# Optimization experiments

Hardware: AMD Instinct MI355X
Metric: run time of the kernel (lower is better)

The kernel has to match this reference:

```python
import jax, jax.numpy as jnp
import numpy as np

B = 8192
D = 512          # hidden_dim
OBS_EMB = 256
COMM = 128
N_ACT = 4
N_LAYERS = 2
D_INNER = 2 * D
D_STATE = 16
DT_RANK = D // 16  # 32
D_CONV = 4
EPS = 1e-5


def _xavier(k, shape):
    s = jnp.sqrt(2.0 / (shape[-2] + shape[-1]))
    return jax.random.normal(k, shape, jnp.float32) * s


def setup_inputs() -> dict:
    ks = jax.random.split(jax.random.key(0), 16)
    p = {}
    p['obs'] = jax.random.normal(ks[0], (B, 75), jnp.float32)
    p['comm_in'] = jax.random.normal(ks[1], (B, COMM), jnp.float32)
    # obs encoder: Conv2d(3->32, k=3, valid) + Linear(288->256)
    p['conv_w'] = jax.random.normal(ks[2], (32, 3, 3, 3), jnp.float32) * jnp.sqrt(2.0 / 27.0)
    p['conv_b'] = jnp.zeros((32,), jnp.float32)
    p['enc_w'] = _xavier(ks[3], (288, OBS_EMB))
    p['enc_b'] = jnp.zeros((OBS_EMB,), jnp.float32)
    p['proj_w'] = _xavier(ks[4], (OBS_EMB + COMM, D))
    p['proj_b'] = jnp.zeros((D,), jnp.float32)
    # Mamba stack params (stacked over layers)
    p['norm_w'] = jnp.ones((N_LAYERS, D), jnp.float32)
    p['in_proj_w'] = _xavier(ks[5], (N_LAYERS, D, 2 * D_INNER))
    p['conv1d_w'] = jax.random.normal(ks[6], (N_LAYERS, D_INNER, D_CONV), jnp.float32) / jnp.sqrt(D_CONV)
    p['conv1d_b'] = jnp.zeros((N_LAYERS, D_INNER), jnp.float32)
    p['x_proj_w'] = _xavier(ks[7], (N_LAYERS, D_INNER, DT_RANK + 2 * D_STATE))
    p['dt_proj_w'] = _xavier(ks[8], (N_LAYERS, DT_RANK, D_INNER))
    p['dt_proj_b'] = jnp.full((N_LAYERS, D_INNER), jnp.log(jnp.expm1(0.01)), jnp.float32)  # dt ~ 0.01
    p['A_log'] = jnp.log(jnp.broadcast_to(jnp.arange(1, D_STATE + 1, dtype=jnp.float32), (N_LAYERS, D_INNER, D_STATE)))
    p['D_param'] = jnp.ones((N_LAYERS, D_INNER), jnp.float32)
    p['out_proj_w'] = _xavier(ks[9], (N_LAYERS, D_INNER, D))
    p['final_norm_w'] = jnp.ones((D,), jnp.float32)
    # output heads
    p['act_w'] = _xavier(ks[10], (D, N_ACT)); p['act_b'] = jnp.zeros((N_ACT,), jnp.float32)
    p['comm_w'] = _xavier(ks[11], (D, COMM)); p['comm_b'] = jnp.zeros((COMM,), jnp.float32)
    p['val_w'] = _xavier(ks[12], (D, 1)); p['val_b'] = jnp.zeros((1,), jnp.float32)
    return p


def _rmsnorm(x, w):
    return x * jax.lax.rsqrt(jnp.mean(x * x, axis=-1, keepdims=True) + EPS) * w


def _mamba_block(u, Wi, cw, cb, Wx, Wdt, bdt, Alog, Dp, Wo):
    # u: (B, L, D) -> (B, L, D)
    Bsz, L, _ = u.shape
    d_inner = Dp.shape[0]
    x, z = jnp.split(u @ Wi, 2, axis=-1)                       # (B,L,di) each
    # causal depthwise conv1d over L
    xt = jnp.pad(jnp.swapaxes(x, 1, 2), ((0, 0), (0, 0), (D_CONV - 1, 0)))
    xc = jax.lax.conv_general_dilated(xt, cw[:, None, :], (1,), 'VALID',
                                      feature_group_count=d_inner,
                                      dimension_numbers=('NCH', 'OIH', 'NCH'))
    x = jax.nn.silu(jnp.swapaxes(xc, 1, 2) + cb)
    x_dbl = x @ Wx                                              # (B,L,dt_rank+2*ns)
    dt = jax.nn.softplus(x_dbl[..., :DT_RANK] @ Wdt + bdt)      # (B,L,di)
    Bm = x_dbl[..., DT_RANK:DT_RANK + D_STATE]                  # (B,L,ns)
    Cm = x_dbl[..., DT_RANK + D_STATE:]                         # (B,L,ns)
    A = -jnp.exp(Alog)                                          # (di,ns)
    dA = jnp.exp(dt[..., None] * A)                             # (B,L,di,ns)
    dBx = dt[..., None] * Bm[:, :, None, :] * x[..., None]      # (B,L,di,ns)

    def step(h, inp):
        dA_t, dBx_t, C_t = inp
        h = dA_t * h + dBx_t
        return h, jnp.einsum('bds,bs->bd', h, C_t)

    h0 = jnp.zeros((Bsz, d_inner, D_STATE), u.dtype)
    _, ys = jax.lax.scan(step, h0, (jnp.swapaxes(dA, 0, 1), jnp.swapaxes(dBx, 0, 1), jnp.swapaxes(Cm, 0, 1)))
    y = jnp.swapaxes(ys, 0, 1) + x * Dp
    return (y * jax.nn.silu(z)) @ Wo


def reference(obs, comm_in, conv_w, conv_b, enc_w, enc_b, proj_w, proj_b,
              norm_w, in_proj_w, conv1d_w, conv1d_b, x_proj_w, dt_proj_w, dt_proj_b,
              A_log, D_param, out_proj_w, final_norm_w,
              act_w, act_b, comm_w, comm_b, val_w, val_b):
    Bsz = obs.shape[0]
    v = obs.reshape(Bsz, 3, 5, 5)
    v = jax.lax.conv_general_dilated(v, conv_w, (1, 1), 'VALID',
                                     dimension_numbers=('NCHW', 'OIHW', 'NCHW'))
    v = jax.nn.relu(v + conv_b[None, :, None, None]).reshape(Bsz, -1)   # (B,288)
    emb = jax.nn.relu(v @ enc_w + enc_b)                                 # (B,256)
    x = jax.nn.relu(jnp.concatenate([emb, comm_in], axis=-1) @ proj_w + proj_b)  # (B,512)
    h = x[:, None, :]                                                    # (B, L=1, D)
    for i in range(norm_w.shape[0]):
        h = h + _mamba_block(_rmsnorm(h, norm_w[i]), in_proj_w[i], conv1d_w[i],
                             conv1d_b[i], x_proj_w[i], dt_proj_w[i], dt_proj_b[i],
                             A_log[i], D_param[i], out_proj_w[i])
    h = _rmsnorm(h, final_norm_w)[:, 0, :]
    action_logits = h @ act_w + act_b
    comm_out = jnp.tanh(h @ comm_w + comm_b)
    value = h @ val_w + val_b
    return action_logits, comm_out, value
```

## Files before the change

### kernel.cpp

```cpp
#include <hip/hip_runtime.h>
#include <math.h>


typedef __bf16 bf16x8 __attribute__((ext_vector_type(8)));
typedef float f32x4 __attribute__((ext_vector_type(4)));
typedef short short8 __attribute__((ext_vector_type(8)));

__device__ __forceinline__ float siluf(float v){ return v / (1.f + __expf(-v)); }
__device__ __forceinline__ float spfast(float v){ return v > 15.f ? v : __logf(1.f + __expf(v)); }
__device__ __forceinline__ float b2f(unsigned short u){ return __uint_as_float(((unsigned)u)<<16); }
__device__ __forceinline__ unsigned short f2b(float f){
  unsigned u = __float_as_uint(f);
  return (unsigned short)((u + 0x7fffu + ((u>>16)&1u)) >> 16);
}
__device__ __forceinline__ void g2l16(const void* g, void* l){
  __builtin_amdgcn_global_load_lds((const __attribute__((address_space(1))) unsigned int*)g,
                                   (__attribute__((address_space(3))) unsigned int*)l, 16, 0, 0);
}
__device__ __forceinline__ float rowscale(const float* ssb, int row){
  return rsqrtf(ssb[row]*(1.f/512.f) + 1e-5f);
}

__global__ __launch_bounds__(256) void k_wt_all(
    const float* __restrict__ in_proj_w, const float* __restrict__ out_proj_w,
    const float* __restrict__ x_proj_w,  const float* __restrict__ dt_proj_w,
    const float* __restrict__ enc_w,     const float* __restrict__ proj_w,
    const float* __restrict__ act_w, const float* __restrict__ comm_w, const float* __restrict__ val_w,
    const float* __restrict__ norm_w, const float* __restrict__ final_nw,
    const float* __restrict__ obs, const float* __restrict__ comm_in,
    const float* __restrict__ conv_w, const float* __restrict__ conv_b,
    unsigned short* __restrict__ wi_t, unsigned short* __restrict__ wo_t,
    unsigned short* __restrict__ wx_t, unsigned short* __restrict__ wdt_t,
    unsigned short* __restrict__ we_t, unsigned short* __restrict__ wp_t,
    unsigned short* __restrict__ wh_t,
    unsigned short* __restrict__ v, unsigned short* __restrict__ cat,
    float* __restrict__ ssbufs )
{
  int b = blockIdx.x;
  const int t = threadIdx.x;

  if (b >= 4816) {
    float4* p = (float4*)(ssbufs + (size_t)(b - 4816)*8192);
    #pragma unroll
    for (int i=0;i<8;i++) p[t + i*256] = (float4){0.f,0.f,0.f,0.f};
    return;
  }
  if (b >= 3792) {
    __shared__ float s_obs[8][76];
    const int r0 = (b - 3792) * 8;
    for (int i = t; i < 8*75; i += 256) s_obs[i/75][i%75] = obs[(size_t)(r0 + i/75)*75 + i%75];
    __syncthreads();
    for (int i = t; i < 8*288; i += 256) {
      int r = i / 288, o = i % 288;
      int c = o / 9, ij = o % 9, oi = ij/3, oj = ij%3;
      float acc = conv_b[c];
      #pragma unroll
      for (int ic=0; ic<3; ic++)
        #pragma unroll
        for (int ki=0; ki<3; ki++)
          #pragma unroll
          for (int kj=0; kj<3; kj++)
            acc = fmaf(s_obs[r][ic*25 + (oi+ki)*5 + (oj+kj)], conv_w[((c*3+ic)*3+ki)*3+kj], acc);
      v[(size_t)(r0+r)*320 + o] = f2b(fmaxf(acc, 0.f));
    }
    v[(size_t)(r0 + (t>>5))*320 + 288 + (t&31)] = 0;
    for (int i = t; i < 8*128; i += 256) {
      int r = i >> 7, c = i & 127;
      cat[(size_t)(r0+r)*384 + 256 + c] = f2b(comm_in[(size_t)(r0+r)*128 + c]);
    }
    return;
  }
  if (b >= 3536) {
    const int n = b - 3536;
    for (int k = t; k < 512; k += 256) {
      float v2;
      if (n < 4)         v2 = act_w[k*4 + n];
      else if (n < 132)  v2 = comm_w[k*128 + (n-4)];
      else if (n == 132) v2 = val_w[k];
      else               v2 = 0.f;
      wh_t[(size_t)n*512 + k] = f2b(v2 * final_nw[k]);
    }
    return;
  }
  const float* Wsrc; unsigned short* Wdst; int Kd, Nd, KP, nkb;
  const float* nwf = nullptr;
  if (b < 2048) {
    const int L = b >> 10; b &= 1023;
    Wsrc = in_proj_w + (size_t)L*512*2048; Wdst = wi_t + (size_t)L*2048*512;
    Kd = 512; Nd = 2048; KP = 512; nkb = 16;
    nwf = norm_w + L*512;
  } else if (b < 3072) {
    b -= 2048; const int L = b >> 9; b &= 511;
    Wsrc = out_proj_w + (size_t)L*1024*512; Wdst = wo_t + (size_t)L*512*1024;
    Kd = 1024; Nd = 512; KP = 1024; nkb = 32;
  } else if (b < 3200) {
    b -= 3072; const int L = b >> 6; b &= 63;
    Wsrc = x_proj_w + (size_t)L*1024*64; Wdst = wx_t + (size_t)L*64*1024;
    Kd = 1024; Nd = 64; KP = 1024; nkb = 32;
  } else if (b < 3264) {
    b -= 3200; const int L = b >> 5; b &= 31;
    Wsrc = dt_proj_w + (size_t)L*32*1024; Wdst = wdt_t + (size_t)L*1024*32;
    Kd = 32; Nd = 1024; KP = 32; nkb = 1;
  } else if (b < 3344) {
    b -= 3264; Wsrc = enc_w; Wdst = we_t; Kd = 288; Nd = 256; KP = 320; nkb = 10;
  } else {
    b -= 3344; Wsrc = proj_w; Wdst = wp_t; Kd = 384; Nd = 512; KP = 384; nkb = 12;
  }
  __shared__ float s[32][33];
  const int kb = (b % nkb)*32, nb = (b / nkb)*32;
  const int c = t & 31, r = t >> 5;
  #pragma unroll
  for (int i=0;i<32;i+=8) {
    const int k = kb + r + i;
    s[r+i][c] = (k < Kd) ? Wsrc[(size_t)k*Nd + nb + c] : 0.f;
  }
  __syncthreads();
  const float nwv = nwf ? nwf[kb + c] : 1.f;
  #pragma unroll
  for (int i=0;i<32;i+=8) Wdst[(size_t)(nb+r+i)*KP + kb + c] = f2b(s[c][r+i] * nwv);
}

template<int K, int NB>
__device__ __forceinline__ void gemmT(const unsigned short* __restrict__ A,
                                      const unsigned short* __restrict__ Bt,
                                      int r0, int c0,
                                      unsigned short* sA, unsigned short* sB,
                                      f32x4 (&acc)[4][NB/32])
{
  constexpr int NF = NB/32;
  constexpr int ABUF = 128*64, BBUF = NB*64;
  const int tid = threadIdx.x;
  const int l = tid & 63;
  const int wr = (tid>>7)&1, wc = (tid>>6)&1;
  const int rowA = tid>>3, kc8 = (tid&7)*8;
  const unsigned short* gA = A  + (size_t)(r0+rowA)*K + kc8;
  const unsigned short* gB = Bt + (size_t)(c0+rowA)*K + kc8;
  const int aOff = (wr*64 + (l&15))*64 + ((l>>4)*8);
  const int bOff = (wc*(NB/2) + (l&15))*64 + ((l>>4)*8);

  auto stage = [&](int kt, int buf) {
    #pragma unroll
    for (int it=0; it<4; ++it)
      g2l16(gA + (size_t)(it*32)*K + kt, sA + buf*ABUF + (it*256+tid)*8);
    #pragma unroll
    for (int it=0; it<NF; ++it)
      g2l16(gB + (size_t)(it*32)*K + kt, sB + buf*BBUF + (it*256+tid)*8);
  };

  stage(0, 0);
  __syncthreads();
  int cur = 0;
  for (int kt=0; kt<K; kt+=64) {
    if (kt + 64 < K) stage(kt + 64, cur ^ 1);
    const unsigned short* pA = sA + cur*ABUF;
    const unsigned short* pB = sB + cur*BBUF;
    #pragma unroll
    for (int ks=0; ks<64; ks+=32) {
      bf16x8 af[4], bfm[NF];
      #pragma unroll
      for (int m=0;m<4;m++) af[m]  = *(const bf16x8*)(pA + (m*16)*64 + aOff + ks);
      #pragma unroll
      for (int n=0;n<NF;n++) bfm[n] = *(const bf16x8*)(pB + (n*16)*64 + bOff + ks);
      #pragma unroll
      for (int m=0;m<4;m++)
        #pragma unroll
        for (int n=0;n<NF;n++)
          acc[m][n] = __builtin_amdgcn_mfma_f32_16x16x32_bf16(af[m], bfm[n], acc[m][n], 0, 0, 0);
    }
    __syncthreads();
    cur ^= 1;
  }
}

__global__ __launch_bounds__(256) void k_gemm_inproj(
    const unsigned short* __restrict__ A, const unsigned short* __restrict__ Bt,
    const float* __restrict__ ssb,
    const float* __restrict__ cw, const float* __restrict__ cb,
    unsigned short* __restrict__ xs, unsigned short* __restrict__ zs)
{
  __shared__ unsigned short sA[2*128*64], sB[2*128*64];
  f32x4 acc[4][4];
  #pragma unroll
  for (int m=0;m<4;m++)
    #pragma unroll
    for (int n=0;n<4;n++) acc[m][n] = (f32x4){0.f,0.f,0.f,0.f};
  const int r0 = blockIdx.x*128, c0 = blockIdx.y*128;
  gemmT<512,128>(A, Bt, r0, c0, sA, sB, acc);

  const int tid = threadIdx.x, l = tid & 63;
  const int wr = (tid>>7)&1, wc = (tid>>6)&1;
  const int colB = c0 + wc*64 + (l&15);
  const int rowB = r0 + wr*64 + ((l>>4)*4);
  float sv[4][4];
  #pragma unroll
  for (int m=0;m<4;m++)
    #pragma unroll
    for (int j=0;j<4;j++) sv[m][j] = rowscale(ssb, rowB + m*16 + j);
  if (c0 < 1024) {
    #pragma unroll
    for (int n=0;n<4;n++){
      const int col = colB + n*16;
      const float cw3 = cw[col*4+3], cbv = cb[col];
      #pragma unroll
      for (int m=0;m<4;m++)
        #pragma unroll
        for (int j=0;j<4;j++){
          const int row = rowB + m*16 + j;
          xs[(size_t)row*1024 + col] = f2b(siluf(fmaf(acc[m][n][j]*sv[m][j], cw3, cbv)));
        }
    }
  } else {
    #pragma unroll
    for (int n=0;n<4;n++){
      const int col = colB + n*16 - 1024;
      #pragma unroll
      for (int m=0;m<4;m++)
        #pragma unroll
        for (int j=0;j<4;j++){
          const int row = rowB + m*16 + j;
          zs[(size_t)row*1024 + col] = f2b(siluf(acc[m][n][j]*sv[m][j]));
        }
    }
  }
}

__global__ __launch_bounds__(256) void k_gemm_outproj(
    const unsigned short* __restrict__ A, const unsigned short* __restrict__ Bt,
    float* __restrict__ h, unsigned short* __restrict__ hb, float* __restrict__ ssb)
{
  __shared__ unsigned short sA[2*128*64], sB[2*64*64];
  f32x4 acc[4][2];
  #pragma unroll
  for (int m=0;m<4;m++)
    #pragma unroll
    for (int n=0;n<2;n++) acc[m][n] = (f32x4){0.f,0.f,0.f,0.f};
  const int r0 = blockIdx.x*128, c0 = blockIdx.y*64;
  gemmT<1024,64>(A, Bt, r0, c0, sA, sB, acc);

  const int tid = threadIdx.x, l = tid & 63;
  const int wr = (tid>>7)&1, wc = (tid>>6)&1;
  const int colB = c0 + wc*32 + (l&15);
  const int rowB = r0 + wr*64 + ((l>>4)*4);
  #pragma unroll
  for (int m=0;m<4;m++)
    #pragma unroll
    for (int j=0;j<4;j++){
      const int row = rowB + m*16 + j;
      float c2 = 0.f;
      #pragma unroll
      for (int n=0;n<2;n++){
        const int col = colB + n*16;
        float hv = h[(size_t)row*512 + col] + acc[m][n][j];
        h[(size_t)row*512 + col] = hv;
        hb[(size_t)row*512 + col] = f2b(hv);
        c2 = fmaf(hv, hv, c2);
      }
      #pragma unroll
      for (int msk=1; msk<16; msk<<=1) c2 += __shfl_xor(c2, msk, 64);
      if ((l & 15) == 0) atomicAdd(&ssb[row], c2);
    }
}

__global__ __launch_bounds__(256) void k_gemm_enc(
    const unsigned short* __restrict__ A, const unsigned short* __restrict__ Bt,
    const float* __restrict__ bias, unsigned short* __restrict__ cat)
{
  __shared__ unsigned short sA[2*128*64], sB[2*64*64];
  f32x4 acc[4][2];
  #pragma unroll
  for (int m=0;m<4;m++)
    #pragma unroll
    for (int n=0;n<2;n++) acc[m][n] = (f32x4){0.f,0.f,0.f,0.f};
  const int r0 = blockIdx.x*128, c0 = blockIdx.y*64;
  gemmT<320,64>(A, Bt, r0, c0, sA, sB, acc);

  const int tid = threadIdx.x, l = tid & 63;
  const int wr = (tid>>7)&1, wc = (tid>>6)&1;
  const int colB = c0 + wc*32 + (l&15);
  const int rowB = r0 + wr*64 + ((l>>4)*4);
  #pragma unroll
  for (int n=0;n<2;n++){
    const int col = colB + n*16;
    const float bv = bias[col];
    #pragma unroll
    for (int m=0;m<4;m++)
      #pragma unroll
      for (int j=0;j<4;j++){
        const size_t row = rowB + m*16 + j;
        cat[row*384 + col] = f2b(fmaxf(acc[m][n][j] + bv, 0.f));
      }
  }
}

__global__ __launch_bounds__(256) void k_gemm_proj(
    const unsigned short* __restrict__ A, const unsigned short* __restrict__ Bt,
    const float* __restrict__ bias, float* __restrict__ h,
    unsigned short* __restrict__ hb, float* __restrict__ ssb)
{
  __shared__ unsigned short sA[2*128*64], sB[2*64*64];
  f32x4 acc[4][2];
  #pragma unroll
  for (int m=0;m<4;m++)
    #pragma unroll
    for (int n=0;n<2;n++) acc[m][n] = (f32x4){0.f,0.f,0.f,0.f};
  const int r0 = blockIdx.x*128, c0 = blockIdx.y*64;
  gemmT<384,64>(A, Bt, r0, c0, sA, sB, acc);

  const int tid = threadIdx.x, l = tid & 63;
  const int wr = (tid>>7)&1, wc = (tid>>6)&1;
  const int colB = c0 + wc*32 + (l&15);
  const int rowB = r0 + wr*64 + ((l>>4)*4);
  #pragma unroll
  for (int m=0;m<4;m++)
    #pragma unroll
    for (int j=0;j<4;j++){
      const int row = rowB + m*16 + j;
      float c2 = 0.f;
      #pragma unroll
      for (int n=0;n<2;n++){
        const int col = colB + n*16;
        float hv = fmaxf(acc[m][n][j] + bias[col], 0.f);
        h[(size_t)row*512 + col] = hv;
        hb[(size_t)row*512 + col] = f2b(hv);
        c2 = fmaf(hv, hv, c2);
      }
      #pragma unroll
      for (int msk=1; msk<16; msk<<=1) c2 += __shfl_xor(c2, msk, 64);
      if ((l & 15) == 0) atomicAdd(&ssb[row], c2);
    }
}

__global__ __launch_bounds__(256) void k_gemm_heads(
    const unsigned short* __restrict__ A, const unsigned short* __restrict__ Bt,
    const float* __restrict__ ssb,
    const float* __restrict__ act_b, const float* __restrict__ comm_b,
    const float* __restrict__ val_b, float* __restrict__ out)
{
  __shared__ unsigned short sA[2*128*64], sB[2*64*64];
  f32x4 acc[4][2];
  #pragma unroll
  for (int m=0;m<4;m++)
    #pragma unroll
    for (int n=0;n<2;n++) acc[m][n] = (f32x4){0.f,0.f,0.f,0.f};
  const int r0 = blockIdx.x*128, c0 = blockIdx.y*64;
  gemmT<512,64>(A, Bt, r0, c0, sA, sB, acc);

  const int tid = threadIdx.x, l = tid & 63;
  const int wr = (tid>>7)&1, wc = (tid>>6)&1;
  const int colB = c0 + wc*32 + (l&15);
  const int rowB = r0 + wr*64 + ((l>>4)*4);
  #pragma unroll
  for (int n=0;n<2;n++){
    const int col = colB + n*16;
    if (col > 132) continue;
    #pragma unroll
    for (int m=0;m<4;m++)
      #pragma unroll
      for (int j=0;j<4;j++){
        const size_t row = rowB + m*16 + j;
        float v = acc[m][n][j] * rowscale(ssb, (int)row);
        if (col < 4)        out[row*4 + col] = v + act_b[col];
        else if (col < 132) out[32768 + row*128 + (col-4)] = tanhf(v + comm_b[col-4]);
        else                out[1081344 + row] = v + val_b[0];
      }
  }
}

__global__ __launch_bounds__(256) void k_ssm_f(
    unsigned short* __restrict__ xs, const unsigned short* __restrict__ zs,
    const unsigned short* __restrict__ Wx_t, const unsigned short* __restrict__ Wdt_t,
    const float* __restrict__ bdt, const float* __restrict__ Dp)
{
  __shared__ unsigned short sX[32*1024];
  __shared__ unsigned short sB[2*64*128];
  __shared__ float s_dbl[32][64];
  __shared__ unsigned short sDt[32*32];
  __shared__ float s_bc[32];
  constexpr int BB = 64*128;
  const int tid = threadIdx.x, l = tid & 63, w = tid >> 6;
  const int r0 = blockIdx.x * 32;

  auto stageWx = [&](int kt, int buf) {
    #pragma unroll
    for (int it=0; it<4; ++it) {
      const int idx = it*256 + tid;
      g2l16(Wx_t + (size_t)(idx>>4)*1024 + (idx&15)*8 + kt, sB + buf*BB + idx*8);
    }
  };

  #pragma unroll
  for (int it=0; it<16; ++it) {
    const int idx = it*256 + tid;
    g2l16(xs + (size_t)(r0 + (idx>>7))*1024 + (idx&127)*8, sX + idx*8);
  }
  stageWx(0, 0);
  __syncthreads();

  f32x4 acc0 = (f32x4){0.f,0.f,0.f,0.f}, acc1 = (f32x4){0.f,0.f,0.f,0.f};
  int cur = 0;
  for (int kt = 0; kt < 1024; kt += 128) {
    if (kt + 128 < 1024) stageWx(kt + 128, cur ^ 1);
    const unsigned short* pB = sB + cur*BB;
    #pragma unroll
    for (int ks=0; ks<128; ks+=32) {
      bf16x8 a0 = *(const bf16x8*)(sX + ((l&15))*1024    + (l>>4)*8 + kt + ks);
      bf16x8 a1 = *(const bf16x8*)(sX + (16+(l&15))*1024 + (l>>4)*8 + kt + ks);
      bf16x8 bf = *(const bf16x8*)(pB + (w*16+(l&15))*128 + (l>>4)*8 + ks);
      acc0 = __builtin_amdgcn_mfma_f32_16x16x32_bf16(a0, bf, acc0, 0, 0, 0);
      acc1 = __builtin_amdgcn_mfma_f32_16x16x32_bf16(a1, bf, acc1, 0, 0, 0);
    }
    __syncthreads();
    cur ^= 1;
  }

  auto stageWdt = [&](int c, int buf) {
    const int cc = c*256;
    #pragma unroll
    for (int it=0; it<4; ++it) {
      const int idx = it*256 + tid;
      g2l16(Wdt_t + (size_t)(cc + (idx>>2))*32 + (idx&3)*8, sB + buf*BB + idx*8);
    }
  };
  stageWdt(0, 0);

  #pragma unroll
  for (int j=0;j<4;j++) {
    s_dbl[(l>>4)*4 + j]     [w*16 + (l&15)] = acc0[j];
    s_dbl[16 + (l>>4)*4 + j][w*16 + (l&15)] = acc1[j];
  }
  __syncthreads();
  if (tid < 32) {
    float a = 0.f;
    #pragma unroll
    for (int s=0;s<16;s++) a = fmaf(s_dbl[tid][32+s], s_dbl[tid][48+s], a);
    s_bc[tid] = a;
  }
  {
    const int r = tid >> 3, c4 = (tid & 7)*4;
    sDt[r*32 + c4]   = f2b(s_dbl[r][c4]);
    sDt[r*32 + c4+1] = f2b(s_dbl[r][c4+1]);
    sDt[r*32 + c4+2] = f2b(s_dbl[r][c4+2]);
    sDt[r*32 + c4+3] = f2b(s_dbl[r][c4+3]);
  }
  __syncthreads();

  bf16x8 af0 = *(const bf16x8*)(sDt + ((l&15))*32    + (l>>4)*8);
  bf16x8 af1 = *(const bf16x8*)(sDt + (16+(l&15))*32 + (l>>4)*8);
  for (int c = 0; c < 4; ++c) {
    if (c + 1 < 4) stageWdt(c + 1, (c + 1) & 1);
    const unsigned short* pB = sB + (c & 1)*BB;
    f32x4 a2[2][4];
    #pragma unroll
    for (int n=0;n<4;n++){
      bf16x8 bn = *(const bf16x8*)(pB + (w*64 + n*16 + (l&15))*32 + (l>>4)*8);
      a2[0][n] = __builtin_amdgcn_mfma_f32_16x16x32_bf16(af0, bn, (f32x4){0.f,0.f,0.f,0.f}, 0, 0, 0);
      a2[1][n] = __builtin_amdgcn_mfma_f32_16x16x32_bf16(af1, bn, (f32x4){0.f,0.f,0.f,0.f}, 0, 0, 0);
    }
    const int cc = c*256;
    #pragma unroll
    for (int n=0;n<4;n++){
      const int col = cc + w*64 + n*16 + (l&15);
      const float bj = bdt[col], dpj = Dp[col];
      #pragma unroll
      for (int m=0;m<2;m++){
        #pragma unroll
        for (int j=0;j<4;j++){
          const int rloc = m*16 + (l>>4)*4 + j;
          const size_t row = r0 + rloc;
          const float dtv = spfast(a2[m][n][j] + bj);
          const float f = fmaf(dtv, s_bc[rloc], dpj);
          const float x = b2f(sX[rloc*1024 + col]);
          const float z = b2f(zs[row*1024 + col]);
          xs[row*1024 + col] = f2b(x * f * z);
        }
      }
    }
    __syncthreads();
  }
}

extern "C" void kernel_launch(void* const* d_in, const int* in_sizes, int n_in,
                              void* d_out, int out_size, void* d_ws, size_t ws_size,
                              hipStream_t stream) {
  const float* obs       = (const float*)d_in[0];
  const float* comm_in   = (const float*)d_in[1];
  const float* conv_w    = (const float*)d_in[2];
  const float* conv_b    = (const float*)d_in[3];
  const float* enc_w     = (const float*)d_in[4];
  const float* enc_b     = (const float*)d_in[5];
  const float* proj_w    = (const float*)d_in[6];
  const float* proj_b    = (const float*)d_in[7];
  const float* norm_w    = (const float*)d_in[8];
  const float* in_proj_w = (const float*)d_in[9];
  const float* conv1d_w  = (const float*)d_in[10];
  const float* conv1d_b  = (const float*)d_in[11];
  const float* x_proj_w  = (const float*)d_in[12];
  const float* dt_proj_w = (const float*)d_in[13];
  const float* dt_proj_b = (const float*)d_in[14];
  const float* D_param   = (const float*)d_in[16];
  const float* out_proj_w= (const float*)d_in[17];
  const float* final_nw  = (const float*)d_in[18];
  const float* act_w     = (const float*)d_in[19];
  const float* act_b     = (const float*)d_in[20];
  const float* comm_w    = (const float*)d_in[21];
  const float* comm_b    = (const float*)d_in[22];
  const float* val_w     = (const float*)d_in[23];
  const float* val_b     = (const float*)d_in[24];
  float* out = (float*)d_out;

  char* W = (char*)d_ws;
  float* h             = (float*)W;
  unsigned short* hb   = (unsigned short*)(W + (16u<<20));
  unsigned short* xs_b = (unsigned short*)(W + (24u<<20));
  unsigned short* zs_b = (unsigned short*)(W + (40u<<20));
  unsigned short* wi_t = (unsigned short*)(W + (56u<<20));
  unsigned short* wo_t = (unsigned short*)(W + (60u<<20));
  float* ssbufs        = (float*)(W + (62u<<20));
  unsigned short* wx_t = (unsigned short*)(W + (64u<<20));
  unsigned short* wdt_t= (unsigned short*)(W + (64u<<20) + (256u<<10));
  unsigned short* wh_t = (unsigned short*)(W + (65u<<20));
  unsigned short* we_t = (unsigned short*)(W + (65u<<20) + (512u<<10));
  unsigned short* wp_t = (unsigned short*)(W + (66u<<20));

  unsigned short* v_b   = xs_b;
  unsigned short* cat_b = zs_b;
  float* ssP = ssbufs;
  float* ss0 = ssbufs + 8192;
  float* ss1 = ssbufs + 16384;

  k_wt_all<<<4819,256,0,stream>>>(in_proj_w, out_proj_w, x_proj_w, dt_proj_w,
                                  enc_w, proj_w, act_w, comm_w, val_w,
                                  norm_w, final_nw,
                                  obs, comm_in, conv_w, conv_b,
                                  wi_t, wo_t, wx_t, wdt_t, we_t, wp_t, wh_t,
                                  v_b, cat_b, ssbufs);

  k_gemm_enc<<<dim3(64,4),256,0,stream>>>(v_b, we_t, enc_b, cat_b);
  k_gemm_proj<<<dim3(64,8),256,0,stream>>>(cat_b, wp_t, proj_b, h, hb, ssP);

  const float* ssin[2] = { ssP, ss0 };
  float* ssout[2] = { ss0, ss1 };
  for (int L=0; L<2; L++) {
    k_gemm_inproj<<<dim3(64,16),256,0,stream>>>(hb, wi_t + (size_t)L*2048*512, ssin[L],
                                                conv1d_w + L*1024*4, conv1d_b + L*1024, xs_b, zs_b);
    k_ssm_f<<<256,256,0,stream>>>(xs_b, zs_b, wx_t + (size_t)L*64*1024,
                                  wdt_t + (size_t)L*1024*32,
                                  dt_proj_b + L*1024, D_param + L*1024);
    k_gemm_outproj<<<dim3(64,8),256,0,stream>>>(xs_b, wo_t + (size_t)L*512*1024, h, hb, ssout[L]);
  }
  k_gemm_heads<<<dim3(64,3),256,0,stream>>>(hb, wh_t, ss1, act_b, comm_b, val_b, out);
}
```

Measured before the change: 240.8 us.

## Drop fp32 residual buffer and widen outproj tiles to 256 rows

The fp32 residual stream h is removed, and the residual is now carried only in bf16 (hb), which is read, updated and rewritten in the outproj epilogue. This removes an fp32 read and write per element in each outproj and the fp32 write in proj. The outproj GEMM is also rewritten as a 512-thread kernel with 256x64 tiles on a 32x8 grid, so each B tile is reused across more rows. In exchange the residual now accumulates in bf16, which loses precision across layers, and the launch has fewer, larger blocks.

```diff
diff --git a/kernel.cpp b/kernel.cpp
--- a/kernel.cpp
+++ b/kernel.cpp
@@ -224,9 +224,81 @@
   }
 }
 
-__global__ __launch_bounds__(256) void k_gemm_outproj(
+__global__ __launch_bounds__(512) void k_gemm_outproj(
     const unsigned short* __restrict__ A, const unsigned short* __restrict__ Bt,
-    float* __restrict__ h, unsigned short* __restrict__ hb, float* __restrict__ ssb)
+    unsigned short* __restrict__ hb, float* __restrict__ ssb)
+{
+  __shared__ unsigned short sA[2*256*64], sB[2*64*64];
+  constexpr int K = 1024, ABUF = 256*64, BBUF = 64*64;
+  f32x4 acc[4][2];
+  #pragma unroll
+  for (int m=0;m<4;m++)
+    #pragma unroll
+    for (int n=0;n<2;n++) acc[m][n] = (f32x4){0.f,0.f,0.f,0.f};
+  const int tid = threadIdx.x, l = tid & 63;
+  const int w = tid >> 6, wr = w >> 1, wc = w & 1;
+  const int r0 = blockIdx.x*256, c0 = blockIdx.y*64;
+  const int rowA = tid>>3, kc8 = (tid&7)*8;
+  const unsigned short* gA = A  + (size_t)(r0+rowA)*K + kc8;
+  const unsigned short* gB = Bt + (size_t)(c0+rowA)*K + kc8;
+  const int aOff = (wr*64 + (l&15))*64 + ((l>>4)*8);
+  const int bOff = (wc*32 + (l&15))*64 + ((l>>4)*8);
+
+  auto stage = [&](int kt, int buf) {
+    #pragma unroll
+    for (int it=0; it<4; ++it)
+      g2l16(gA + (size_t)(it*64)*K + kt, sA + buf*ABUF + (it*512+tid)*8);
+    g2l16(gB + kt, sB + buf*BBUF + tid*8);
+  };
+
+  stage(0, 0);
+  __syncthreads();
+  int cur = 0;
+  for (int kt=0; kt<K; kt+=64) {
+    if (kt + 64 < K) stage(kt + 64, cur ^ 1);
+    const unsigned short* pA = sA + cur*ABUF;
+    const unsigned short* pB = sB + cur*BBUF;
+    #pragma unroll
+    for (int ks=0; ks<64; ks+=32) {
+      bf16x8 af[4], bfm[2];
+      #pragma unroll
+      for (int m=0;m<4;m++) af[m]  = *(const bf16x8*)(pA + (m*16)*64 + aOff + ks);
+      #pragma unroll
+      for (int n=0;n<2;n++) bfm[n] = *(const bf16x8*)(pB + (n*16)*64 + bOff + ks);
+      #pragma unroll
+      for (int m=0;m<4;m++)
+        #pragma unroll
+        for (int n=0;n<2;n++)
+          acc[m][n] = __builtin_amdgcn_mfma_f32_16x16x32_bf16(af[m], bfm[n], acc[m][n], 0, 0, 0);
+    }
+    __syncthreads();
+    cur ^= 1;
+  }
+
+  const int colB = c0 + wc*32 + (l&15);
+  const int rowB = r0 + wr*64 + ((l>>4)*4);
+  #pragma unroll
+  for (int m=0;m<4;m++)
+    #pragma unroll
+    for (int j=0;j<4;j++){
+      const int row = rowB + m*16 + j;
+      float c2 = 0.f;
+      #pragma unroll
+      for (int n=0;n<2;n++){
+        const int col = colB + n*16;
+        float hv = b2f(hb[(size_t)row*512 + col]) + acc[m][n][j];
+        hb[(size_t)row*512 + col] = f2b(hv);
+        c2 = fmaf(hv, hv, c2);
+      }
+      #pragma unroll
+      for (int msk=1; msk<16; msk<<=1) c2 += __shfl_xor(c2, msk, 64);
+      if ((l & 15) == 0) atomicAdd(&ssb[row], c2);
+    }
+}
+
+__global__ __launch_bounds__(256) void k_gemm_enc(
+    const unsigned short* __restrict__ A, const unsigned short* __restrict__ Bt,
+    const float* __restrict__ bias, unsigned short* __restrict__ cat)
 {
   __shared__ unsigned short sA[2*128*64], sB[2*64*64];
   f32x4 acc[4][2];
@@ -235,35 +307,30 @@
     #pragma unroll
     for (int n=0;n<2;n++) acc[m][n] = (f32x4){0.f,0.f,0.f,0.f};
   const int r0 = blockIdx.x*128, c0 = blockIdx.y*64;
-  gemmT<1024,64>(A, Bt, r0, c0, sA, sB, acc);
+  gemmT<320,64>(A, Bt, r0, c0, sA, sB, acc);
 
   const int tid = threadIdx.x, l = tid & 63;
   const int wr = (tid>>7)&1, wc = (tid>>6)&1;
   const int colB = c0 + wc*32 + (l&15);
   const int rowB = r0 + wr*64 + ((l>>4)*4);
   #pragma unroll
-  for (int m=0;m<4;m++)
-    #pragma unroll
-    for (int j=0;j<4;j++){
-      const int row = rowB + m*16 + j;
-      float c2 = 0.f;
-      #pragma unroll
-      for (int n=0;n<2;n++){
-        const int col = colB + n*16;
-        float hv = h[(size_t)row*512 + col] + acc[m][n][j];
-        h[(size_t)row*512 + col] = hv;
-        hb[(size_t)row*512 + col] = f2b(hv);
-        c2 = fmaf(hv, hv, c2);
+  for (int n=0;n<2;n++){
+    const int col = colB + n*16;
+    const float bv = bias[col];
+    #pragma unroll
+    for (int m=0;m<4;m++)
+      #pragma unroll
+      for (int j=0;j<4;j++){
+        const size_t row = rowB + m*16 + j;
+        cat[row*384 + col] = f2b(fmaxf(acc[m][n][j] + bv, 0.f));
       }
-      #pragma unroll
-      for (int msk=1; msk<16; msk<<=1) c2 += __shfl_xor(c2, msk, 64);
-      if ((l & 15) == 0) atomicAdd(&ssb[row], c2);
-    }
-}
-
-__global__ __launch_bounds__(256) void k_gemm_enc(
+  }
+}
+
+__global__ __launch_bounds__(256) void k_gemm_proj(
     const unsigned short* __restrict__ A, const unsigned short* __restrict__ Bt,
-    const float* __restrict__ bias, unsigned short* __restrict__ cat)
+    const float* __restrict__ bias,
+    unsigned short* __restrict__ hb, float* __restrict__ ssb)
 {
   __shared__ unsigned short sA[2*128*64], sB[2*64*64];
   f32x4 acc[4][2];
@@ -272,45 +339,13 @@
     #pragma unroll
     for (int n=0;n<2;n++) acc[m][n] = (f32x4){0.f,0.f,0.f,0.f};
   const int r0 = blockIdx.x*128, c0 = blockIdx.y*64;
-  gemmT<320,64>(A, Bt, r0, c0, sA, sB, acc);
+  gemmT<384,64>(A, Bt, r0, c0, sA, sB, acc);
 
   const int tid = threadIdx.x, l = tid & 63;
   const int wr = (tid>>7)&1, wc = (tid>>6)&1;
   const int colB = c0 + wc*32 + (l&15);
   const int rowB = r0 + wr*64 + ((l>>4)*4);
   #pragma unroll
-  for (int n=0;n<2;n++){
-    const int col = colB + n*16;
-    const float bv = bias[col];
-    #pragma unroll
-    for (int m=0;m<4;m++)
-      #pragma unroll
-      for (int j=0;j<4;j++){
-        const size_t row = rowB + m*16 + j;
-        cat[row*384 + col] = f2b(fmaxf(acc[m][n][j] + bv, 0.f));
-      }
-  }
-}
-
-__global__ __launch_bounds__(256) void k_gemm_proj(
-    const unsigned short* __restrict__ A, const unsigned short* __restrict__ Bt,
-    const float* __restrict__ bias, float* __restrict__ h,
-    unsigned short* __restrict__ hb, float* __restrict__ ssb)
-{
-  __shared__ unsigned short sA[2*128*64], sB[2*64*64];
-  f32x4 acc[4][2];
-  #pragma unroll
-  for (int m=0;m<4;m++)
-    #pragma unroll
-    for (int n=0;n<2;n++) acc[m][n] = (f32x4){0.f,0.f,0.f,0.f};
-  const int r0 = blockIdx.x*128, c0 = blockIdx.y*64;
-  gemmT<384,64>(A, Bt, r0, c0, sA, sB, acc);
-
-  const int tid = threadIdx.x, l = tid & 63;
-  const int wr = (tid>>7)&1, wc = (tid>>6)&1;
-  const int colB = c0 + wc*32 + (l&15);
-  const int rowB = r0 + wr*64 + ((l>>4)*4);
-  #pragma unroll
   for (int m=0;m<4;m++)
     #pragma unroll
     for (int j=0;j<4;j++){
@@ -320,7 +355,6 @@
       for (int n=0;n<2;n++){
         const int col = colB + n*16;
         float hv = fmaxf(acc[m][n][j] + bias[col], 0.f);
-        h[(size_t)row*512 + col] = hv;
         hb[(size_t)row*512 + col] = f2b(hv);
         c2 = fmaf(hv, hv, c2);
       }
@@ -509,7 +543,6 @@
   float* out = (float*)d_out;
 
   char* W = (char*)d_ws;
-  float* h             = (float*)W;
   unsigned short* hb   = (unsigned short*)(W + (16u<<20));
   unsigned short* xs_b = (unsigned short*)(W + (24u<<20));
   unsigned short* zs_b = (unsigned short*)(W + (40u<<20));
@@ -536,7 +569,7 @@
                                   v_b, cat_b, ssbufs);
 
   k_gemm_enc<<<dim3(64,4),256,0,stream>>>(v_b, we_t, enc_b, cat_b);
-  k_gemm_proj<<<dim3(64,8),256,0,stream>>>(cat_b, wp_t, proj_b, h, hb, ssP);
+  k_gemm_proj<<<dim3(64,8),256,0,stream>>>(cat_b, wp_t, proj_b, hb, ssP);
 
   const float* ssin[2] = { ssP, ss0 };
   float* ssout[2] = { ss0, ss1 };
@@ -546,7 +579,7 @@
     k_ssm_f<<<256,256,0,stream>>>(xs_b, zs_b, wx_t + (size_t)L*64*1024,
                                   wdt_t + (size_t)L*1024*32,
                                   dt_proj_b + L*1024, D_param + L*1024);
-    k_gemm_outproj<<<dim3(64,8),256,0,stream>>>(xs_b, wo_t + (size_t)L*512*1024, h, hb, ssout[L]);
+    k_gemm_outproj<<<dim3(32,8),512,0,stream>>>(xs_b, wo_t + (size_t)L*512*1024, hb, ssout[L]);
   }
   k_gemm_heads<<<dim3(64,3),256,0,stream>>>(hb, wh_t, ss1, act_b, comm_b, val_b, out);
 }
```

After: 246.2 us. 2.3% more time.
